# Kernel tuning notes

Measured on AMD Instinct MI355X. Metric: run time of the kernel, lower is better.

## Reference

```python
import jax, jax.numpy as jnp
import numpy as np

B, N = 2, 6
H, W = 64, 64            # BEV grid
FH, FW = 32, 88          # camera feature map
DIM, FEAT_DIM = 128, 128
HEADS, DH = 4, 32
QW1, QW2 = 8, 8          # query window
KW1, KW2 = 4, 11         # key/val window
IMG_H, IMG_W = 224, 480
EPS = 1e-5


def _ln(t, g, b):
    m = t.mean(-1, keepdims=True)
    v = ((t - m) ** 2).mean(-1, keepdims=True)
    return (t - m) / jnp.sqrt(v + EPS) * g + b


def _bn_relu_conv(t, g, b, Wc):
    # eval-mode BatchNorm2d (running_mean=0, running_var=1) -> ReLU -> 1x1 conv
    y = jax.nn.relu(t / jnp.sqrt(1.0 + EPS) * g[:, None, None] + b[:, None, None])
    return jnp.einsum('oc,nchw->nohw', Wc, y)


def _normalize(t, axis):
    n = jnp.sqrt(jnp.sum(t * t, axis=axis, keepdims=True))
    return t / jnp.maximum(n, 1e-12)


def _win(t, w1, w2):
    # (..., X*w1, Y*w2, d) -> (..., X, Y, w1, w2, d)
    s = t.shape
    t = t.reshape(*s[:-3], s[-3] // w1, w1, s[-2] // w2, w2, s[-1])
    return jnp.swapaxes(t, -4, -3)


def _unwin(t):
    # (..., X, Y, w1, w2, d) -> (..., X*w1, Y*w2, d)
    s = t.shape
    return jnp.swapaxes(t, -4, -3).reshape(*s[:-5], s[-5] * s[-3], s[-4] * s[-2], s[-1])


def _gridwin(t, w1, w2):
    bb, nn, Ht, Wt, d = t.shape
    t = t.reshape(bb, nn, w1, Ht // w1, w2, Wt // w2, d)
    return t.transpose(0, 1, 3, 5, 2, 4, 6)  # (b, n, X, Y, w1, w2, d)


def _cross_win_attn(qw, kw, vw, ln_g, ln_b, Wqkv, bqkv, Wp, bp, skip):
    b, n, X, Y, w1, w2, d = qw.shape
    f1, f2 = kw.shape[4], kw.shape[5]
    L = X * Y
    q = qw.transpose(0, 2, 3, 1, 4, 5, 6).reshape(b, L, n * w1 * w2, d)
    k = kw.transpose(0, 2, 3, 1, 4, 5, 6).reshape(b, L, n * f1 * f2, d)
    v = vw.transpose(0, 2, 3, 1, 4, 5, 6).reshape(b, L, n * f1 * f2, d)
    q = _ln(q, ln_g[0], ln_b[0]) @ Wqkv[0] + bqkv[0]
    k = _ln(k, ln_g[1], ln_b[1]) @ Wqkv[1] + bqkv[1]
    v = _ln(v, ln_g[2], ln_b[2]) @ Wqkv[2] + bqkv[2]
    split = lambda t: t.reshape(*t.shape[:-1], HEADS, DH)  # head-major channel split
    q, k, v = split(q), split(k), split(v)
    att = jax.nn.softmax(DH ** -0.5 * jnp.einsum('blqhd,blkhd->bhlqk', q, k), axis=-1)
    o = jnp.einsum('bhlqk,blkhd->blqhd', att, v).reshape(b, L, n * w1 * w2, HEADS * DH)
    o = o @ Wp + bp
    o = o.reshape(b, X, Y, n, w1, w2, d).mean(3)  # mean over cameras
    return o + skip


def _forward(x, grid, feature, I_inv, E_inv,
             bn_fl_g, bn_fl_b, W_fl, bn_fp_g, bn_fp_b, W_fp,
             W_bev, b_bev, W_img, W_cam,
             attn_ln_g, attn_ln_b, attn_Wqkv, attn_bqkv, attn_Wp, attn_bp,
             pn_g, pn_b, Wma, bma, Wmb, bmb, post_g, post_b):
    b, n = feature.shape[:2]
    # image plane (buffer)
    xs = jnp.linspace(0.0, 1.0, FW) * IMG_W
    ys = jnp.linspace(0.0, 1.0, FH) * IMG_H
    gx, gy = jnp.meshgrid(xs, ys)  # (FH, FW) each
    plane = jnp.stack([gx, gy, jnp.ones_like(gx)], 0).reshape(3, FH * FW)
    # camera embedding from translation column of E_inv
    c = E_inv[..., -1]                                   # (b, n, 4)
    c_embed = jnp.einsum('oc,bnc->bno', W_cam, c)        # (b, n, dim)
    # unprojected rays
    cam = jnp.einsum('bnij,jk->bnik', I_inv, plane)      # (b, n, 3, HW)
    cam = jnp.concatenate([cam, jnp.ones_like(cam[:, :, :1])], 2)
    d = jnp.einsum('bnij,bnjk->bnik', E_inv, cam)        # (b, n, 4, HW)
    d_img = d.reshape(b, n, 4, FH, FW)
    d_embed = jnp.einsum('oc,bnchw->bnohw', W_img, d_img)
    img_embed = _normalize(d_embed - c_embed[..., None, None], axis=2)
    # BEV positional embedding
    w_embed = jnp.einsum('oc,chw->ohw', W_bev, grid[:2]) + b_bev[:, None, None]
    bev_embed = _normalize(w_embed[None, None] - c_embed[..., None, None], axis=2)  # (b,n,dim,H,W)
    feat = feature.reshape(b * n, FEAT_DIM, FH, FW)
    key_im = img_embed + _bn_relu_conv(feat, bn_fp_g, bn_fp_b, W_fp).reshape(b, n, DIM, FH, FW)
    val_im = _bn_relu_conv(feat, bn_fl_g, bn_fl_b, W_fl).reshape(b, n, DIM, FH, FW)
    query = bev_embed + x[:, None]                       # (b, n, dim, H, W)
    # channel-last
    q_im = query.transpose(0, 1, 3, 4, 2)
    k_im = key_im.transpose(0, 1, 3, 4, 2)
    v_im = val_im.transpose(0, 1, 3, 4, 2)
    x_im = x.transpose(0, 2, 3, 1)
    # stage 1: local windows
    qw = _win(q_im, QW1, QW2)
    kw = _win(k_im, KW1, KW2)
    vw = _win(v_im, KW1, KW2)
    o1 = _cross_win_attn(qw, kw, vw, attn_ln_g[0], attn_ln_b[0], attn_Wqkv[0],
                         attn_bqkv[0], attn_Wp[0], attn_bp[0], _win(x_im, QW1, QW2))
    q1 = _unwin(o1)                                      # (b, H, W, d)
    q1 = q1 + jax.nn.gelu(_ln(q1, pn_g[0], pn_b[0]) @ Wma[0] + bma[0], approximate=False) @ Wmb[0] + bmb[0]
    # stage 2: grid (swapped) windows
    qg = jnp.broadcast_to(q1[:, None], (b, n) + q1.shape[1:])
    o2 = _cross_win_attn(_win(qg, QW1, QW2), _gridwin(k_im, KW1, KW2), _gridwin(v_im, KW1, KW2),
                         attn_ln_g[1], attn_ln_b[1], attn_Wqkv[1], attn_bqkv[1],
                         attn_Wp[1], attn_bp[1], _win(q1, QW1, QW2))
    q2 = _unwin(o2)
    q2 = q2 + jax.nn.gelu(_ln(q2, pn_g[1], pn_b[1]) @ Wma[1] + bma[1], approximate=False) @ Wmb[1] + bmb[1]
    out = _ln(q2, post_g, post_b)
    return out.transpose(0, 3, 1, 2)                     # (b, dim, H, W)


def setup_inputs() -> dict:
    key = jax.random.key(0)
    ks = jax.random.split(key, 16)
    rn = lambda i, shape, sc=0.02: jax.random.normal(ks[i], shape, dtype=jnp.float32) * sc
    return {
        'index': 0,
        'x': jax.random.normal(ks[0], (B, DIM, H, W), dtype=jnp.float32),
        'grid': jax.random.normal(ks[1], (2, H, W), dtype=jnp.float32),
        'feature': jax.random.normal(ks[2], (B, N, FEAT_DIM, FH, FW), dtype=jnp.float32),
        'I_inv': jax.random.normal(ks[3], (B, N, 3, 3), dtype=jnp.float32),
        'E_inv': jax.random.normal(ks[4], (B, N, 4, 4), dtype=jnp.float32),
        'bn_fl_g': jnp.ones((FEAT_DIM,), jnp.float32), 'bn_fl_b': jnp.zeros((FEAT_DIM,), jnp.float32),
        'W_fl': rn(5, (DIM, FEAT_DIM)),
        'bn_fp_g': jnp.ones((FEAT_DIM,), jnp.float32), 'bn_fp_b': jnp.zeros((FEAT_DIM,), jnp.float32),
        'W_fp': rn(6, (DIM, FEAT_DIM)),
        'W_bev': rn(7, (DIM, 2)), 'b_bev': jnp.zeros((DIM,), jnp.float32),
        'W_img': rn(8, (DIM, 4)), 'W_cam': rn(9, (DIM, 4)),
        'attn_ln_g': jnp.ones((2, 3, DIM), jnp.float32), 'attn_ln_b': jnp.zeros((2, 3, DIM), jnp.float32),
        'attn_Wqkv': rn(10, (2, 3, DIM, HEADS * DH)), 'attn_bqkv': jnp.zeros((2, 3, HEADS * DH), jnp.float32),
        'attn_Wp': rn(11, (2, HEADS * DH, DIM)), 'attn_bp': jnp.zeros((2, DIM), jnp.float32),
        'pn_g': jnp.ones((2, DIM), jnp.float32), 'pn_b': jnp.zeros((2, DIM), jnp.float32),
        'Wma': rn(12, (2, DIM, 2 * DIM)), 'bma': jnp.zeros((2, 2 * DIM), jnp.float32),
        'Wmb': rn(13, (2, 2 * DIM, DIM)), 'bmb': jnp.zeros((2, DIM), jnp.float32),
        'post_g': jnp.ones((DIM,), jnp.float32), 'post_b': jnp.zeros((DIM,), jnp.float32),
    }


def reference(index, x, grid, feature, I_inv, E_inv,
              bn_fl_g, bn_fl_b, W_fl, bn_fp_g, bn_fp_b, W_fp,
              W_bev, b_bev, W_img, W_cam,
              attn_ln_g, attn_ln_b, attn_Wqkv, attn_bqkv, attn_Wp, attn_bp,
              pn_g, pn_b, Wma, bma, Wmb, bmb, post_g, post_b):
    del index  # grid for this index is passed directly
    return _forward(x, grid, feature, I_inv, E_inv,
                    bn_fl_g, bn_fl_b, W_fl, bn_fp_g, bn_fp_b, W_fp,
                    W_bev, b_bev, W_img, W_cam,
                    attn_ln_g, attn_ln_b, attn_Wqkv, attn_bqkv, attn_Wp, attn_bp,
                    pn_g, pn_b, Wma, bma, Wmb, bmb, post_g, post_b)
```

## Files before the change

kernel.cpp:

```cpp
#include <hip/hip_runtime.h>
#include <math.h>


typedef __attribute__((ext_vector_type(8))) short short8;
typedef __attribute__((ext_vector_type(4))) float f32x4;

__device__ __forceinline__ unsigned short f2bf(float f){
  union { float f; unsigned u; } v; v.f = f;
  unsigned r = v.u + 0x7FFF + ((v.u >> 16) & 1);
  return (unsigned short)(r >> 16);
}
__device__ __forceinline__ float bf2f(unsigned short h){
  union { unsigned u; float f; } v; v.u = ((unsigned)h) << 16; return v.f;
}
__device__ __forceinline__ void store_bf16x8(unsigned short* p, const float* v){
  union { short8 s8; unsigned short u[8]; } u;
  #pragma unroll
  for (int i=0;i<8;i++) u.u[i] = f2bf(v[i]);
  *(short8*)p = u.s8;
}

__device__ __forceinline__ float gelu_erf(float x){
  float z = x * 0.70710678118654752f;
  float a = fabsf(z);
  float t = 1.0f / fmaf(0.3275911f, a, 1.0f);
  float p = t*(0.254829592f + t*(-0.284496736f + t*(1.421413741f +
            t*(-1.453152027f + t*1.061405429f))));
  float er = 1.0f - p*__expf(-a*a);
  er = copysignf(er, z);
  return 0.5f * x * (1.0f + er);
}

__device__ __forceinline__ size_t remap_kv(int tok, int mode){
  int bn = tok / 2816; int p = tok - bn*2816;
  int b = bn / 6, n = bn - b*6;
  int i = p / 88, j = p - i*88;
  int l, t;
  if (mode == 1){
    int jw = j / 11;
    l = (i >> 2)*8 + jw;
    t = n*44 + (i & 3)*11 + (j - jw*11);
  } else {
    l = (i & 7)*8 + (j & 7);
    t = n*44 + (i >> 3)*11 + (j >> 3);
  }
  return (size_t)((b*64 + l)*264 + t);
}

__global__ __launch_bounds__(256) void k_prepconv(
    const float* __restrict__ qkv, const float* __restrict__ wp,
    const float* __restrict__ wma, const float* __restrict__ wmb,
    unsigned short* __restrict__ Wt,
    const float* __restrict__ abqkv, float* __restrict__ biasP,
    const float* __restrict__ gridp, const float* __restrict__ Wbev,
    const float* __restrict__ bbev, const float* __restrict__ x,
    const float* __restrict__ lg, const float* __restrict__ lb,
    const float* __restrict__ Einv, const float* __restrict__ Wcam,
    unsigned short* __restrict__ Qh,
    const float* __restrict__ feat,
    const float* __restrict__ gfp, const float* __restrict__ bfp,
    const float* __restrict__ Wfp,
    const float* __restrict__ gfl, const float* __restrict__ bfl,
    const float* __restrict__ Wfl,
    const float* __restrict__ Iinv, const float* __restrict__ Wimg,
    unsigned short* __restrict__ K1h, unsigned short* __restrict__ V1h){
  constexpr int KP_ = 136;
  __shared__ unsigned short sW[128*KP_];
  __shared__ unsigned short sA[128*KP_];
  __shared__ float sg_[128], sb_[128];
  __shared__ float sMean[128], sRstd[128], sRn[128];
  __shared__ float sCE[128];
  __shared__ float4 sWI4[128];
  __shared__ float sIE[32];
  const int bid = blockIdx.x;
  const int tid = threadIdx.x;

  if (bid < 56){
    const int sel[14]  = {0,0,0,0,0,0, 1,1, 2,2, 3,3,3,3};
    const int soff[14] = {0,16384,32768,49152,65536,81920, 0,16384, 0,32768,
                          0,16384,32768,49152};
    const int doff[14] = {0,16384,32768,49152,65536,81920, 98304,114688,
                          131072,163840, 196608,212992,229376,245760};
    const int Ns[14]   = {128,128,128,128,128,128, 128,128, 256,256,
                          128,128,128,128};
    int sg = bid >> 2, q = bid & 3;
    const float* srcs[4] = {qkv, wp, wma, wmb};
    const float* src = srcs[sel[sg]] + soff[sg];
    unsigned short* dst = Wt + doff[sg];
    int K = 128, N = Ns[sg];
    int quarter = (K*N) >> 2;
    bool fold = (sg >= 1 && sg <= 5);
    const float* gv = lg + sg*128;
    for (int idx = q*quarter + tid; idx < (q+1)*quarter; idx += 256){
      int n = idx / K, k = idx - n*K;
      float v = src[k*N + n];
      if (fold) v *= gv[k];
      dst[idx] = f2bf(v);
    }
  } else if (bid < 62){
    if (tid < 128){
      int m = bid - 56;
      int n = tid;
      float s = abqkv[m*128 + n];
      if (m > 0){
        const float* lnb = lb + m*128;
        const float* W = qkv + m*16384;
        for (int k=0;k<128;k++) s = fmaf(lnb[k], W[k*128 + n], s);
      }
      biasP[m*128 + n] = s;
    }
  } else if (bid < 574){
    float* sx = (float*)sW;
    int bid2 = bid - 62;
    int b = bid2 >> 8; int pp0 = (bid2 & 255) << 4;
    {
      int cg = tid >> 4, px = tid & 15;
      #pragma unroll
      for (int i=0;i<8;i++){
        int c = cg + 16*i;
        sx[c*17 + px] = x[(size_t)b*524288 + (size_t)c*4096 + pp0 + px];
      }
    }
    __syncthreads();
    int xid = tid >> 4, part = tid & 15;
    int pix = pp0 + xid;
    int h = pix >> 6, w = pix & 63;
    int l = (h>>3)*8 + (w>>3);
    int tq = (h&7)*8 + (w&7);
    float g0 = gridp[pix], g1 = gridp[4096 + pix];
    float we[8], xv[8];
    #pragma unroll
    for (int k=0;k<8;k++){
      int o = part*8 + k;
      we[k] = Wbev[o*2]*g0 + Wbev[o*2+1]*g1 + bbev[o];
      xv[k] = sx[(part*8+k)*17 + xid];
    }
    for (int n=0; n<6; n++){
      const float* E = Einv + (b*6+n)*16;
      float v[8]; float sq = 0.f;
      #pragma unroll
      for (int k=0;k<8;k++){
        int o = part*8 + k;
        const float* Wc = Wcam + o*4;
        float ce = Wc[0]*E[3] + Wc[1]*E[7] + Wc[2]*E[11] + Wc[3]*E[15];
        float vv = we[k] - ce;
        v[k] = vv; sq = fmaf(vv, vv, sq);
      }
      #pragma unroll
      for (int off=8; off>0; off>>=1) sq += __shfl_xor(sq, off, 16);
      float rn = 1.0f / fmaxf(sqrtf(sq), 1e-12f);
      float q[8]; float s=0.f, s2=0.f;
      #pragma unroll
      for (int k=0;k<8;k++){
        q[k] = fmaf(v[k], rn, xv[k]);
        s += q[k]; s2 = fmaf(q[k], q[k], s2);
      }
      #pragma unroll
      for (int off=8; off>0; off>>=1){ s += __shfl_xor(s, off, 16); s2 += __shfl_xor(s2, off, 16); }
      float mean = s*(1.f/128.f);
      float rstd = rsqrtf(fmaxf(s2*(1.f/128.f) - mean*mean, 0.f) + 1e-5f);
      size_t row = (size_t)((b*64 + l)*384 + n*64 + tq);
      float o8[8];
      #pragma unroll
      for (int k=0;k<8;k++){
        int c = part*8 + k;
        o8[k] = fmaf((q[k]-mean)*rstd, lg[c], lb[c]);
      }
      store_bf16x8(Qh + row*128 + part*8, o8);
    }
  } else {
    const int bid2c = bid - 574;
    const int which = (bid2c >= 264);
    const int cbid = which ? bid2c - 264 : bid2c;
    const float* gg = which ? gfl : gfp;
    const float* bb = which ? bfl : bfp;
    const float* Wf = which ? Wfl : Wfp;
    unsigned short* OUT = which ? V1h : K1h;
    const int base = cbid * 128;
    const int bn = base / 2816;
    const int pbase = base - bn*2816;
    for (int i = tid; i < 2048; i += 256){
      int n = i >> 4, k8 = (i & 15) << 3;
      const float* wsp = Wf + (size_t)n*128 + k8;
      float4 f0 = *(const float4*)wsp;
      float4 f1 = *(const float4*)(wsp+4);
      float v8[8] = {f0.x,f0.y,f0.z,f0.w,f1.x,f1.y,f1.z,f1.w};
      store_bf16x8(&sW[n*KP_ + k8], v8);
    }
    if (tid < 128){ sg_[tid]=gg[tid]; sb_[tid]=bb[tid]; }
    if (!which){
      if (tid < 128){
        const float* E = Einv + bn*16;
        float4 wc = *(const float4*)(Wcam + tid*4);
        sCE[tid] = wc.x*E[3] + wc.y*E[7] + wc.z*E[11] + wc.w*E[15];
        sWI4[tid] = *(const float4*)(Wimg + tid*4);
      }
      if (tid < 25) sIE[tid] = (tid < 9) ? Iinv[bn*9 + tid] : Einv[bn*16 + (tid-9)];
    }
    const float RSQ = rsqrtf(1.0f + 1e-5f);
    {
      int prow = tid & 127, cseg = tid >> 7;
      int p = pbase + prow;
      const float* fb = feat + ((size_t)bn*128 + cseg*64)*2816 + p;
      #pragma unroll 8
      for (int i=0;i<64;i+=2){
        int c = cseg*64 + i;
        float t0 = fb[(size_t)i*2816] * RSQ;
        float t1 = fb[(size_t)(i+1)*2816] * RSQ;
        float y0 = fmaxf(fmaf(t0, sg_[c],   sb_[c]),   0.f);
        float y1 = fmaxf(fmaf(t1, sg_[c+1], sb_[c+1]), 0.f);
        unsigned u = (unsigned)f2bf(y0) | ((unsigned)f2bf(y1) << 16);
        *(unsigned*)&sA[prow*KP_ + c] = u;
      }
    }
    __syncthreads();
    const int lane = tid & 63, wv = tid >> 6;
    const int lane15 = lane & 15, quad = lane >> 4;
    const int n0 = wv * 32;
    f32x4 acc[8][2];
    #pragma unroll
    for (int mt=0; mt<8; mt++){ acc[mt][0]=(f32x4)0.f; acc[mt][1]=(f32x4)0.f; }
    const unsigned short* aptr = sA + lane15*KP_ + quad*8;
    const unsigned short* bptr = sW + (size_t)(n0 + lane15)*KP_ + quad*8;
    #pragma unroll
    for (int kk=0; kk<4; kk++){
      short8 af[8], bf2v[2];
      #pragma unroll
      for (int mt=0; mt<8; mt++) af[mt] = *(const short8*)(aptr + mt*16*KP_ + kk*32);
      bf2v[0] = *(const short8*)(bptr + kk*32);
      bf2v[1] = *(const short8*)(bptr + 16*KP_ + kk*32);
      #pragma unroll
      for (int mt=0; mt<8; mt++){
        acc[mt][0] = __builtin_amdgcn_mfma_f32_16x16x32_bf16(af[mt], bf2v[0], acc[mt][0], 0,0,0);
        acc[mt][1] = __builtin_amdgcn_mfma_f32_16x16x32_bf16(af[mt], bf2v[1], acc[mt][1], 0,0,0);
      }
    }
    __syncthreads();
    if (!which){
      const int r = tid >> 1, half = tid & 1;
      int p = pbase + r;
      int ii = p / 88, jj = p - ii*88;
      float xs = (float)jj * (480.0f/87.0f);
      float ys = (float)ii * (224.0f/31.0f);
      float c0 = sIE[0]*xs + sIE[1]*ys + sIE[2];
      float c1 = sIE[3]*xs + sIE[4]*ys + sIE[5];
      float c2 = sIE[6]*xs + sIE[7]*ys + sIE[8];
      float d0 = sIE[9]*c0  + sIE[10]*c1 + sIE[11]*c2 + sIE[12];
      float d1 = sIE[13]*c0 + sIE[14]*c1 + sIE[15]*c2 + sIE[16];
      float d2 = sIE[17]*c0 + sIE[18]*c1 + sIE[19]*c2 + sIE[20];
      float d3 = sIE[21]*c0 + sIE[22]*c1 + sIE[23]*c2 + sIE[24];
      float sq = 0.f;
      #pragma unroll 8
      for (int k=0;k<64;k++){
        int c = half*64 + k;
        float4 w = sWI4[c];
        float de = w.x*d0 + w.y*d1 + w.z*d2 + w.w*d3 - sCE[c];
        sA[r*KP_ + c] = f2bf(de);
        sq = fmaf(de, de, sq);
      }
      sq += __shfl_xor(sq, 1);
      if (half == 0) sRn[r] = 1.0f / fmaxf(sqrtf(sq), 1e-12f);
    }
    __syncthreads();
    #pragma unroll
    for (int mt=0; mt<8; mt++){
      #pragma unroll
      for (int nt=0; nt<2; nt++){
        int col = n0 + nt*16 + lane15;
        #pragma unroll
        for (int r4=0; r4<4; r4++){
          int row = mt*16 + quad*4 + r4;
          float v = acc[mt][nt][r4];
          if (!which) v += bf2f(sA[row*KP_ + col]) * sRn[row];
          sA[row*KP_ + col] = f2bf(v);
        }
      }
    }
    __syncthreads();
    {
      int r = tid >> 1, part = tid & 1;
      float s=0.f, s2=0.f;
      #pragma unroll 8
      for (int k=0;k<64;k++){
        float v = bf2f(sA[r*KP_ + part*64 + k]);
        s += v; s2 = fmaf(v,v,s2);
      }
      s += __shfl_xor(s, 1); s2 += __shfl_xor(s2, 1);
      if (part == 0){
        float mean = s*(1.f/128.f);
        sMean[r] = mean;
        sRstd[r] = rsqrtf(fmaxf(s2*(1.f/128.f) - mean*mean, 0.f) + 1e-5f);
      }
    }
    __syncthreads();
    for (int i = tid; i < 2048; i += 256){
      int row = i >> 4, seg = i & 15;
      float mean = sMean[row], rstd = sRstd[row];
      union { short8 s; unsigned short u[8]; } t;
      t.s = *(const short8*)&sA[row*KP_ + seg*8];
      float v[8];
      #pragma unroll
      for (int k=0;k<8;k++) v[k] = (bf2f(t.u[k]) - mean)*rstd;
      store_bf16x8(OUT + (size_t)(base+row)*128 + seg*8, v);
    }
  }
}

struct GArg {
  const unsigned short* Xh;
  const unsigned short* Wt; const float* bias;
  unsigned short* OUTH; float oscale; int outmode;
};
struct G5 { GArg g[5]; int s[4]; };

__global__ __launch_bounds__(256) void k_qkv5(G5 A){
  constexpr int KP_ = 136;
  __shared__ unsigned short sW[128*KP_];
  __shared__ unsigned short sA[128*KP_];
  __shared__ float sbias[128];
  const int b0 = (int)blockIdx.x;
  const int ridx = (b0 < A.s[0]) ? 0 : (b0 < A.s[1]) ? 1 : (b0 < A.s[2]) ? 2
                 : (b0 < A.s[3]) ? 3 : 4;
  const GArg g = A.g[ridx];
  const int bid = b0 - (ridx ? A.s[ridx-1] : 0);
  const int base = bid * 128;
  const int tid = threadIdx.x;
  for (int i = tid; i < 2048; i += 256){
    int n = i >> 4, k8 = (i & 15) << 3;
    *(short8*)&sW[n*KP_ + k8] = *(const short8*)(g.Wt + (size_t)n*128 + k8);
  }
  if (tid < 128) sbias[tid] = g.bias[tid];
  {
    const int r = tid >> 1, part = tid & 1;
    const short8* src = (const short8*)(g.Xh + (size_t)(base+r)*128 + part*64);
    short8* dst = (short8*)(sA + r*KP_ + part*64);
    #pragma unroll
    for (int k=0;k<8;k++) dst[k] = src[k];
  }
  __syncthreads();
  const int lane = tid & 63, wv = tid >> 6;
  const int lane15 = lane & 15, quad = lane >> 4;
  const int n0 = wv * 32;
  f32x4 acc[8][2];
  #pragma unroll
  for (int mt=0; mt<8; mt++){ acc[mt][0]=(f32x4)0.f; acc[mt][1]=(f32x4)0.f; }
  const unsigned short* aptr = sA + lane15*KP_ + quad*8;
  const unsigned short* bptr = sW + (size_t)(n0 + lane15)*KP_ + quad*8;
  #pragma unroll
  for (int kk=0; kk<4; kk++){
    short8 af[8], bf2v[2];
    #pragma unroll
    for (int mt=0; mt<8; mt++) af[mt] = *(const short8*)(aptr + mt*16*KP_ + kk*32);
    bf2v[0] = *(const short8*)(bptr + kk*32);
    bf2v[1] = *(const short8*)(bptr + 16*KP_ + kk*32);
    #pragma unroll
    for (int mt=0; mt<8; mt++){
      acc[mt][0] = __builtin_amdgcn_mfma_f32_16x16x32_bf16(af[mt], bf2v[0], acc[mt][0], 0,0,0);
      acc[mt][1] = __builtin_amdgcn_mfma_f32_16x16x32_bf16(af[mt], bf2v[1], acc[mt][1], 0,0,0);
    }
  }
  __syncthreads();
  #pragma unroll
  for (int mt=0; mt<8; mt++){
    #pragma unroll
    for (int nt=0; nt<2; nt++){
      int col = n0 + nt*16 + lane15;
      float bsv = sbias[col];
      #pragma unroll
      for (int r4=0; r4<4; r4++){
        int row = mt*16 + quad*4 + r4;
        sA[row*KP_ + col] = f2bf((acc[mt][nt][r4] + bsv) * g.oscale);
      }
    }
  }
  __syncthreads();
  for (int i = tid; i < 2048; i += 256){
    int row = i >> 4, seg = i & 15;
    int rrow = base + row;
    size_t orow = g.outmode ? remap_kv(rrow, g.outmode) : (size_t)rrow;
    *(short8*)(g.OUTH + orow*128 + seg*8) = *(const short8*)&sA[row*KP_ + seg*8];
  }
}

__global__ __launch_bounds__(256) void k_tail(
    const unsigned short* __restrict__ AOh,
    const float* __restrict__ skipf, int skipmode,
    const unsigned short* __restrict__ WtP, const float* __restrict__ abp,
    const float* __restrict__ png, const float* __restrict__ pnb,
    const unsigned short* __restrict__ WtMAa, const unsigned short* __restrict__ WtMAb,
    const float* __restrict__ bma,
    const unsigned short* __restrict__ WtMBa, const unsigned short* __restrict__ WtMBb,
    const float* __restrict__ bmb,
    float* __restrict__ Q1out,
    const unsigned short* __restrict__ WtQ2, const float* __restrict__ q2bias,
    float q2scale, unsigned short* __restrict__ QPout,
    const float* __restrict__ postg, const float* __restrict__ postb,
    float* __restrict__ out){
  constexpr int KP_ = 136;
  __shared__ unsigned short sW[128*KP_];
  __shared__ unsigned short sX[32*KP_];
  __shared__ unsigned short sH1[32*KP_];
  __shared__ unsigned short sH2[32*KP_];
  __shared__ float sCUR[32*132];
  __shared__ float sbias[128];
  __shared__ float sg[128], sb2[128];
  __shared__ float sMean[32], sRstd[32];
  const int tid = threadIdx.x;
  const int base = blockIdx.x * 32;
  const int lane = tid & 63, wv = tid >> 6;
  const int lane15 = lane & 15, quad = lane >> 4;
  const int n0 = wv * 32;

  auto loadW = [&](const unsigned short* Wp){
    for (int i = tid; i < 2048; i += 256){
      int n = i >> 4, k8 = (i & 15) << 3;
      *(short8*)&sW[n*KP_ + k8] = *(const short8*)(Wp + (size_t)n*128 + k8);
    }
  };
  auto domfma = [&](const unsigned short* Asrc, f32x4 acc[2][2]){
    const unsigned short* aptr = Asrc + lane15*KP_ + quad*8;
    const unsigned short* bptr = sW + (size_t)(n0 + lane15)*KP_ + quad*8;
    #pragma unroll
    for (int kk=0; kk<4; kk++){
      short8 a0 = *(const short8*)(aptr + kk*32);
      short8 a1 = *(const short8*)(aptr + 16*KP_ + kk*32);
      short8 b0 = *(const short8*)(bptr + kk*32);
      short8 b1 = *(const short8*)(bptr + 16*KP_ + kk*32);
      acc[0][0] = __builtin_amdgcn_mfma_f32_16x16x32_bf16(a0,b0,acc[0][0],0,0,0);
      acc[1][0] = __builtin_amdgcn_mfma_f32_16x16x32_bf16(a1,b0,acc[1][0],0,0,0);
      acc[0][1] = __builtin_amdgcn_mfma_f32_16x16x32_bf16(a0,b1,acc[0][1],0,0,0);
      acc[1][1] = __builtin_amdgcn_mfma_f32_16x16x32_bf16(a1,b1,acc[1][1],0,0,0);
    }
  };

  loadW(WtP);
  {
    const int r = tid >> 3, part = tid & 7;
    const short8* src = (const short8*)(AOh + (size_t)(base+r)*128 + part*16);
    short8* dst = (short8*)(sX + r*KP_ + part*16);
    dst[0] = src[0]; dst[1] = src[1];
  }
  if (tid < 128){ sbias[tid] = abp[tid]; sg[tid] = png[tid]; sb2[tid] = pnb[tid]; }
  __syncthreads();
  {
    f32x4 acc[2][2];
    acc[0][0]=(f32x4)0.f; acc[0][1]=(f32x4)0.f;
    acc[1][0]=(f32x4)0.f; acc[1][1]=(f32x4)0.f;
    domfma(sX, acc);
    #pragma unroll
    for (int mt=0; mt<2; mt++)
      #pragma unroll
      for (int nt=0; nt<2; nt++){
        int col = n0 + nt*16 + lane15;
        float bsv = sbias[col];
        #pragma unroll
        for (int r4=0; r4<4; r4++){
          int row = mt*16 + quad*4 + r4;
          int rrow = base + row;
          float v = acc[mt][nt][r4] + bsv;
          if (skipmode == 1){
            int bb = rrow >> 12, l = (rrow >> 6) & 63, pp = rrow & 63;
            int pix = (((l>>3)*8 + (pp>>3)) << 6) + (l&7)*8 + (pp&7);
            v += skipf[(size_t)bb*524288 + (size_t)col*4096 + pix];
          } else {
            v += skipf[(size_t)rrow*128 + col];
          }
          sCUR[row*132 + col] = v;
        }
      }
  }
  __syncthreads();
  loadW(WtMAa);
  if (tid < 128) sbias[tid] = bma[tid];
  {
    const int r = tid >> 3, part = tid & 7;
    float v[16];
    #pragma unroll
    for (int k=0;k<16;k++) v[k] = sCUR[r*132 + part*16 + k];
    float s=0.f, s2=0.f;
    #pragma unroll
    for (int k=0;k<16;k++){ s += v[k]; s2 = fmaf(v[k],v[k],s2); }
    #pragma unroll
    for (int off=4; off>0; off>>=1){ s += __shfl_xor(s, off, 8); s2 += __shfl_xor(s2, off, 8); }
    float mean = s*(1.f/128.f);
    float rstd = rsqrtf(fmaxf(s2*(1.f/128.f) - mean*mean, 0.f) + 1e-5f);
    #pragma unroll
    for (int k=0;k<16;k++){
      int c = part*16 + k;
      v[k] = fmaf((v[k]-mean)*rstd, sg[c], sb2[c]);
    }
    store_bf16x8(sX + r*KP_ + part*16, v);
    store_bf16x8(sX + r*KP_ + part*16 + 8, v+8);
  }
  __syncthreads();
  {
    f32x4 acc[2][2];
    acc[0][0]=(f32x4)0.f; acc[0][1]=(f32x4)0.f;
    acc[1][0]=(f32x4)0.f; acc[1][1]=(f32x4)0.f;
    domfma(sX, acc);
    #pragma unroll
    for (int mt=0; mt<2; mt++)
      #pragma unroll
      for (int nt=0; nt<2; nt++){
        int col = n0 + nt*16 + lane15;
        float bsv = sbias[col];
        #pragma unroll
        for (int r4=0; r4<4; r4++){
          int row = mt*16 + quad*4 + r4;
          sH1[row*KP_ + col] = f2bf(gelu_erf(acc[mt][nt][r4] + bsv));
        }
      }
  }
  __syncthreads();
  loadW(WtMAb);
  if (tid < 128) sbias[tid] = bma[128 + tid];
  __syncthreads();
  {
    f32x4 acc[2][2];
    acc[0][0]=(f32x4)0.f; acc[0][1]=(f32x4)0.f;
    acc[1][0]=(f32x4)0.f; acc[1][1]=(f32x4)0.f;
    domfma(sX, acc);
    #pragma unroll
    for (int mt=0; mt<2; mt++)
      #pragma unroll
      for (int nt=0; nt<2; nt++){
        int col = n0 + nt*16 + lane15;
        float bsv = sbias[col];
        #pragma unroll
        for (int r4=0; r4<4; r4++){
          int row = mt*16 + quad*4 + r4;
          sH2[row*KP_ + col] = f2bf(gelu_erf(acc[mt][nt][r4] + bsv));
        }
      }
  }
  __syncthreads();
  loadW(WtMBa);
  if (tid < 128) sbias[tid] = bmb[tid];
  __syncthreads();
  f32x4 acc[2][2];
  acc[0][0]=(f32x4)0.f; acc[0][1]=(f32x4)0.f;
  acc[1][0]=(f32x4)0.f; acc[1][1]=(f32x4)0.f;
  domfma(sH1, acc);
  __syncthreads();
  loadW(WtMBb);
  __syncthreads();
  domfma(sH2, acc);
  if (out == nullptr){
    #pragma unroll
    for (int mt=0; mt<2; mt++)
      #pragma unroll
      for (int nt=0; nt<2; nt++){
        int col = n0 + nt*16 + lane15;
        float bsv = sbias[col];
        #pragma unroll
        for (int r4=0; r4<4; r4++){
          int row = mt*16 + quad*4 + r4;
          float v = acc[mt][nt][r4] + bsv + sCUR[row*132 + col];
          sCUR[row*132 + col] = v;
          Q1out[(size_t)(base+row)*128 + col] = v;
        }
      }
    __syncthreads();
    {
      const int r = tid >> 3, part = tid & 7;
      float s=0.f, s2=0.f;
      #pragma unroll
      for (int k=0;k<16;k++){
        float v = sCUR[r*132 + part*16 + k];
        s += v; s2 = fmaf(v,v,s2);
      }
      #pragma unroll
      for (int off=4; off>0; off>>=1){ s += __shfl_xor(s, off, 8); s2 += __shfl_xor(s2, off, 8); }
      if (part == 0){
        float mean = s*(1.f/128.f);
        sMean[r] = mean;
        sRstd[r] = rsqrtf(fmaxf(s2*(1.f/128.f) - mean*mean, 0.f) + 1e-5f);
      }
    }
    __syncthreads();
    {
      const int r = tid >> 3, part = tid & 7;
      float mean = sMean[r], rstd = sRstd[r];
      float v[16];
      #pragma unroll
      for (int k=0;k<16;k++) v[k] = (sCUR[r*132 + part*16 + k] - mean)*rstd;
      store_bf16x8(sX + r*KP_ + part*16, v);
      store_bf16x8(sX + r*KP_ + part*16 + 8, v+8);
    }
    loadW(WtQ2);
    if (tid < 128) sbias[tid] = q2bias[tid];
    __syncthreads();
    f32x4 a2[2][2];
    a2[0][0]=(f32x4)0.f; a2[0][1]=(f32x4)0.f;
    a2[1][0]=(f32x4)0.f; a2[1][1]=(f32x4)0.f;
    domfma(sX, a2);
    #pragma unroll
    for (int mt=0; mt<2; mt++)
      #pragma unroll
      for (int nt=0; nt<2; nt++){
        int col = n0 + nt*16 + lane15;
        float bsv = sbias[col];
        #pragma unroll
        for (int r4=0; r4<4; r4++){
          int row = mt*16 + quad*4 + r4;
          sH1[row*KP_ + col] = f2bf((a2[mt][nt][r4] + bsv) * q2scale);
        }
      }
    __syncthreads();
    for (int i = tid; i < 512; i += 256){
      int row = i >> 4, seg = i & 15;
      *(short8*)(QPout + (size_t)(base+row)*128 + seg*8) = *(const short8*)&sH1[row*KP_ + seg*8];
    }
  } else {
    float res[2][2][4];
    #pragma unroll
    for (int mt=0; mt<2; mt++)
      #pragma unroll
      for (int nt=0; nt<2; nt++){
        int col = n0 + nt*16 + lane15;
        float bsv = sbias[col];
        #pragma unroll
        for (int r4=0; r4<4; r4++){
          int row = mt*16 + quad*4 + r4;
          res[mt][nt][r4] = acc[mt][nt][r4] + bsv + sCUR[row*132 + col];
        }
      }
    __syncthreads();
    #pragma unroll
    for (int mt=0; mt<2; mt++)
      #pragma unroll
      for (int nt=0; nt<2; nt++){
        int col = n0 + nt*16 + lane15;
        #pragma unroll
        for (int r4=0; r4<4; r4++){
          int row = mt*16 + quad*4 + r4;
          sCUR[row*132 + col] = res[mt][nt][r4];
        }
      }
    __syncthreads();
    {
      const int r = tid >> 3, part = tid & 7;
      float s=0.f, s2=0.f;
      #pragma unroll
      for (int k=0;k<16;k++){
        float v = sCUR[r*132 + part*16 + k];
        s += v; s2 = fmaf(v,v,s2);
      }
      #pragma unroll
      for (int off=4; off>0; off>>=1){ s += __shfl_xor(s, off, 8); s2 += __shfl_xor(s2, off, 8); }
      if (part == 0){
        float mean = s*(1.f/128.f);
        sMean[r] = mean;
        sRstd[r] = rsqrtf(fmaxf(s2*(1.f/128.f) - mean*mean, 0.f) + 1e-5f);
      }
    }
    __syncthreads();
    {
      int c = tid & 127, half = tid >> 7;
      int b = base >> 12, l = (base >> 6) & 63, p0 = base & 63;
      float go = postg[c], bo = postb[c];
      #pragma unroll
      for (int seg=0; seg<2; seg++){
        int p = p0 + half*16 + seg*8;
        int hrow = (l>>3)*8 + (p>>3);
        int w0 = (l&7)*8;
        float rr[8];
        #pragma unroll
        for (int j=0;j<8;j++){
          int row = half*16 + seg*8 + j;
          rr[j] = fmaf((sCUR[row*132 + c] - sMean[row])*sRstd[row], go, bo);
        }
        size_t obase = ((size_t)(b*128 + c))*4096 + (size_t)hrow*64 + w0;
        *(float4*)&out[obase]   = make_float4(rr[0],rr[1],rr[2],rr[3]);
        *(float4*)&out[obase+4] = make_float4(rr[4],rr[5],rr[6],rr[7]);
      }
    }
  }
}

__global__ __launch_bounds__(256) void k_attn2(const unsigned short* __restrict__ QPh,
    const unsigned short* __restrict__ KPh, const unsigned short* __restrict__ VPh,
    unsigned short* __restrict__ AOh, int nrep, int nQ){
  __shared__ unsigned short Ksh[288*40];
  __shared__ unsigned short Vt[32*296];
  __shared__ unsigned short Psh[4*16*40];
  __shared__ float rs[4*16];
  int hd = blockIdx.x & 3; int bl = blockIdx.x >> 2;
  size_t kvbase = (size_t)bl*264;
  int tid = threadIdx.x;
  for (int idx = tid; idx < 1056; idx += 256){
    int row = idx >> 2, seg = idx & 3;
    *(short8*)&Ksh[row*40 + seg*8] =
      *(const short8*)(KPh + (kvbase+row)*128 + hd*32 + seg*8);
  }
  for (int idx = tid; idx < 96; idx += 256){
    int row = 264 + (idx>>2), seg = idx & 3;
    short8 z = {0,0,0,0,0,0,0,0};
    *(short8*)&Ksh[row*40 + seg*8] = z;
  }
  for (int idx = tid; idx < 528; idx += 256){
    int kp = idx >> 2, seg = idx & 3;
    union { short8 s; unsigned short u[8]; } a, b;
    a.s = *(const short8*)(VPh + (kvbase + 2*kp)*128 + hd*32 + seg*8);
    b.s = *(const short8*)(VPh + (kvbase + 2*kp + 1)*128 + hd*32 + seg*8);
    #pragma unroll
    for (int i=0;i<8;i++)
      *(unsigned*)&Vt[(seg*8+i)*296 + 2*kp] = (unsigned)a.u[i] | ((unsigned)b.u[i] << 16);
  }
  for (int idx = tid; idx < 384; idx += 256){
    int d = idx / 12, kp = 264 + (idx % 12)*2;
    *(unsigned*)&Vt[d*296 + kp] = 0u;
  }
  __syncthreads();
  const int wv = tid >> 6, lane = tid & 63;
  const int lane15 = lane & 15, quad = lane >> 4;
  unsigned short* Pw = Psh + wv*640;
  float* rsw = rs + wv*16;
  short8 vfrag[9][2];
  #pragma unroll
  for (int kc=0; kc<9; kc++){
    vfrag[kc][0] = *(const short8*)&Vt[(lane15)*296      + kc*32 + quad*8];
    vfrag[kc][1] = *(const short8*)&Vt[(16+lane15)*296   + kc*32 + quad*8];
  }
  f32x4 macc0 = (f32x4)0.f, macc1 = (f32x4)0.f;
  for (int cam = 0; cam < nrep; cam++){
    int qrow = bl*nQ + (cam*4 + wv)*16 + lane15;
    short8 qf = *(const short8*)(QPh + (size_t)qrow*128 + hd*32 + quad*8);
    f32x4 oa0 = (f32x4)0.f, oa1 = (f32x4)0.f;
    float rsum = 0.f;
    #pragma unroll
    for (int kc=0; kc<9; kc++){
      #pragma unroll
      for (int sub=0; sub<2; sub++){
        int kt = kc*2 + sub;
        short8 kf = *(const short8*)&Ksh[(kt*16 + lane15)*40 + quad*8];
        f32x4 st = __builtin_amdgcn_mfma_f32_16x16x32_bf16(kf, qf, (f32x4)0.f, 0,0,0);
        int kbase = kt*16 + quad*4;
        float e0 = (kbase+0 < 264) ? __expf(st[0]) : 0.f;
        float e1 = (kbase+1 < 264) ? __expf(st[1]) : 0.f;
        float e2 = (kbase+2 < 264) ? __expf(st[2]) : 0.f;
        float e3 = (kbase+3 < 264) ? __expf(st[3]) : 0.f;
        rsum += (e0+e1)+(e2+e3);
        uint2 pk;
        pk.x = (unsigned)f2bf(e0) | ((unsigned)f2bf(e1) << 16);
        pk.y = (unsigned)f2bf(e2) | ((unsigned)f2bf(e3) << 16);
        *(uint2*)&Pw[lane15*40 + sub*16 + quad*4] = pk;
      }
      short8 pf = *(const short8*)&Pw[lane15*40 + quad*8];
      oa0 = __builtin_amdgcn_mfma_f32_16x16x32_bf16(pf, vfrag[kc][0], oa0, 0,0,0);
      oa1 = __builtin_amdgcn_mfma_f32_16x16x32_bf16(pf, vfrag[kc][1], oa1, 0,0,0);
    }
    rsum += __shfl_xor(rsum, 16);
    rsum += __shfl_xor(rsum, 32);
    if (lane < 16) rsw[lane] = rsum;
    f32x4 rv = *(f32x4*)&rsw[quad*4];
    #pragma unroll
    for (int r=0;r<4;r++){
      float inv = 1.f / rv[r];
      macc0[r] = fmaf(oa0[r], inv, macc0[r]);
      macc1[r] = fmaf(oa1[r], inv, macc1[r]);
    }
  }
  float sc = (nrep == 6) ? (1.f/6.f) : 1.f;
  int pixb = wv*16 + quad*4;
  #pragma unroll
  for (int r=0;r<4;r++){
    size_t rowo = ((size_t)(bl*64 + pixb + r))*128 + hd*32;
    AOh[rowo + lane15]      = f2bf(macc0[r]*sc);
    AOh[rowo + 16 + lane15] = f2bf(macc1[r]*sc);
  }
}

extern "C" void kernel_launch(void* const* d_in, const int* in_sizes, int n_in,
                              void* d_out, int out_size, void* d_ws, size_t ws_size,
                              hipStream_t stream) {
  (void)in_sizes; (void)n_in; (void)out_size; (void)ws_size;
  const float* x     = (const float*)d_in[1];
  const float* gridp = (const float*)d_in[2];
  const float* feat  = (const float*)d_in[3];
  const float* Iinv  = (const float*)d_in[4];
  const float* Einv  = (const float*)d_in[5];
  const float* gfl   = (const float*)d_in[6];
  const float* bfl   = (const float*)d_in[7];
  const float* Wfl   = (const float*)d_in[8];
  const float* gfp   = (const float*)d_in[9];
  const float* bfp   = (const float*)d_in[10];
  const float* Wfp   = (const float*)d_in[11];
  const float* Wbev  = (const float*)d_in[12];
  const float* bbev  = (const float*)d_in[13];
  const float* Wimg  = (const float*)d_in[14];
  const float* Wcam  = (const float*)d_in[15];
  const float* alng  = (const float*)d_in[16];
  const float* alnb  = (const float*)d_in[17];
  const float* aWqkv = (const float*)d_in[18];
  const float* abqkv = (const float*)d_in[19];
  const float* aWp   = (const float*)d_in[20];
  const float* abp   = (const float*)d_in[21];
  const float* png   = (const float*)d_in[22];
  const float* pnb   = (const float*)d_in[23];
  const float* Wma   = (const float*)d_in[24];
  const float* bma   = (const float*)d_in[25];
  const float* Wmb   = (const float*)d_in[26];
  const float* bmb   = (const float*)d_in[27];
  const float* postg = (const float*)d_in[28];
  const float* postb = (const float*)d_in[29];
  float* out = (float*)d_out;
  float* ws  = (float*)d_ws;
  const float QSC = 0.17677669529663687f;

  float* biasP = ws;
  unsigned short* Wt   = (unsigned short*)(ws + 2048);
  unsigned short* K1h  = (unsigned short*)(ws + 149504);
  unsigned short* V1h  = K1h + 4325376;
  unsigned short* KPh  = V1h + 4325376;
  unsigned short* VPh  = KPh + 4325376;
  unsigned short* KP2h = VPh + 4325376;
  unsigned short* VP2h = KP2h + 4325376;
  unsigned short* QPh  = VP2h + 4325376;
  unsigned short* Qbh  = QPh + 6291456;
  unsigned short* AOh  = Qbh + 6291456;
  float* Q1f = (float*)(AOh + 1048576);

  unsigned short* WtQ1 = Wt;            unsigned short* WtK1 = Wt + 16384;
  unsigned short* WtV1 = Wt + 32768;    unsigned short* WtQ2 = Wt + 49152;
  unsigned short* WtK2 = Wt + 65536;    unsigned short* WtV2 = Wt + 81920;
  unsigned short* WtP1 = Wt + 98304;    unsigned short* WtP2 = Wt + 114688;
  unsigned short* WtMA1 = Wt + 131072;  unsigned short* WtMA2 = Wt + 163840;
  unsigned short* WtMB1a = Wt + 196608; unsigned short* WtMB1b = Wt + 212992;
  unsigned short* WtMB2a = Wt + 229376; unsigned short* WtMB2b = Wt + 245760;

  k_prepconv<<<1102, 256, 0, stream>>>(aWqkv, aWp, Wma, Wmb, Wt,
      abqkv, biasP, gridp, Wbev, bbev, x, alng, alnb, Einv, Wcam, Qbh,
      feat, gfp, bfp, Wfp, gfl, bfl, Wfl, Iinv, Wimg, K1h, V1h);

  {
    G5 A;
    A.g[0] = GArg{Qbh, WtQ1, biasP,      QPh,  QSC, 0};
    A.g[1] = GArg{K1h, WtK1, biasP+128,  KPh,  1.f, 1};
    A.g[2] = GArg{V1h, WtV1, biasP+256,  VPh,  1.f, 1};
    A.g[3] = GArg{K1h, WtK2, biasP+512,  KP2h, 1.f, 2};
    A.g[4] = GArg{V1h, WtV2, biasP+640,  VP2h, 1.f, 2};
    A.s[0] = 384; A.s[1] = 648; A.s[2] = 912; A.s[3] = 1176;
    k_qkv5<<<1440, 256, 0, stream>>>(A);
  }
  k_attn2<<<512, 256, 0, stream>>>(QPh, KPh, VPh, AOh, 6, 384);
  k_tail<<<256, 256, 0, stream>>>(AOh, x, 1, WtP1, abp, png, pnb,
      WtMA1, WtMA1+16384, bma, WtMB1a, WtMB1b, bmb, Q1f,
      WtQ2, biasP+384, QSC, QPh,
      nullptr, nullptr, nullptr);
  k_attn2<<<512, 256, 0, stream>>>(QPh, KP2h, VP2h, AOh, 1, 64);
  k_tail<<<256, 256, 0, stream>>>(AOh, Q1f, 3, WtP2, abp+128, png+128, pnb+128,
      WtMA2, WtMA2+16384, bma+256, WtMB2a, WtMB2b, bmb+128, nullptr,
      nullptr, nullptr, 0.f, nullptr,
      postg, postb, out);
}
```

Baseline: 254.1 us.

## Fuse Q projection into prep kernel and share K/V tile across two projections

The first-stage Q projection GEMM moves into the prep kernel. Each block converts the Q weight to bf16 in shared memory and runs MFMA on its 96 freshly normalized query rows, so the Qbh intermediate is no longer written to and read back from global memory. The K/V projection kernel now loads each K1/V1 tile once and applies both the stage-1 and stage-2 weights to it, halving activation reads and block count. The cost is that every prep block re-converts the full 128x128 fp32 weight, and the prep blocks carry more shared memory and registers.

Measured after the change: 255.8 us. About the same (+0.7%).

```diff
diff --git a/kernel.cpp b/kernel.cpp
--- a/kernel.cpp
+++ b/kernel.cpp
@@ -56,7 +56,7 @@
     const float* __restrict__ bbev, const float* __restrict__ x,
     const float* __restrict__ lg, const float* __restrict__ lb,
     const float* __restrict__ Einv, const float* __restrict__ Wcam,
-    unsigned short* __restrict__ Qh,
+    unsigned short* __restrict__ QPh,
     const float* __restrict__ feat,
     const float* __restrict__ gfp, const float* __restrict__ bfp,
     const float* __restrict__ Wfp,
@@ -67,21 +67,17 @@
   constexpr int KP_ = 136;
   __shared__ unsigned short sW[128*KP_];
   __shared__ unsigned short sA[128*KP_];
-  __shared__ float sg_[128], sb_[128];
-  __shared__ float sMean[128], sRstd[128], sRn[128];
-  __shared__ float sCE[128];
-  __shared__ float4 sWI4[128];
-  __shared__ float sIE[32];
+  __shared__ __align__(16) float sMisc[2560];
   const int bid = blockIdx.x;
   const int tid = threadIdx.x;
 
-  if (bid < 56){
-    const int sel[14]  = {0,0,0,0,0,0, 1,1, 2,2, 3,3,3,3};
-    const int soff[14] = {0,16384,32768,49152,65536,81920, 0,16384, 0,32768,
+  if (bid < 52){
+    const int sel[13]  = {0,0,0,0,0, 1,1, 2,2, 3,3,3,3};
+    const int soff[13] = {16384,32768,49152,65536,81920, 0,16384, 0,32768,
                           0,16384,32768,49152};
-    const int doff[14] = {0,16384,32768,49152,65536,81920, 98304,114688,
+    const int doff[13] = {16384,32768,49152,65536,81920, 98304,114688,
                           131072,163840, 196608,212992,229376,245760};
-    const int Ns[14]   = {128,128,128,128,128,128, 128,128, 256,256,
+    const int Ns[13]   = {128,128,128,128,128, 128,128, 256,256,
                           128,128,128,128};
     int sg = bid >> 2, q = bid & 3;
     const float* srcs[4] = {qkv, wp, wma, wmb};
@@ -89,17 +85,17 @@
     unsigned short* dst = Wt + doff[sg];
     int K = 128, N = Ns[sg];
     int quarter = (K*N) >> 2;
-    bool fold = (sg >= 1 && sg <= 5);
-    const float* gv = lg + sg*128;
+    bool fold = (sg <= 4);
+    const float* gv = lg + (sg+1)*128;
     for (int idx = q*quarter + tid; idx < (q+1)*quarter; idx += 256){
       int n = idx / K, k = idx - n*K;
       float v = src[k*N + n];
       if (fold) v *= gv[k];
       dst[idx] = f2bf(v);
     }
-  } else if (bid < 62){
+  } else if (bid < 58){
     if (tid < 128){
-      int m = bid - 56;
+      int m = bid - 52;
       int n = tid;
       float s = abqkv[m*128 + n];
       if (m > 0){
@@ -109,10 +105,16 @@
       }
       biasP[m*128 + n] = s;
     }
-  } else if (bid < 574){
-    float* sx = (float*)sW;
-    int bid2 = bid - 62;
+  } else if (bid < 570){
+    const float QSCALE = 0.17677669529663687f;
+    float* sx = sMisc;
+    int* rowoff = (int*)(sMisc + 2176);
+    int bid2 = bid - 58;
     int b = bid2 >> 8; int pp0 = (bid2 & 255) << 4;
+    for (int idx = tid; idx < 16384; idx += 256){
+      int n = idx & 127, k = idx >> 7;
+      sW[n*KP_ + k] = f2bf(qkv[(size_t)k*128 + n]);
+    }
     {
       int cg = tid >> 4, px = tid & 15;
       #pragma unroll
@@ -121,12 +123,14 @@
         sx[c*17 + px] = x[(size_t)b*524288 + (size_t)c*4096 + pp0 + px];
       }
     }
+    if (tid < 16){
+      int pix = pp0 + tid; int h = pix >> 6, w = pix & 63;
+      int l = (h>>3)*8 + (w>>3); int tq = (h&7)*8 + (w&7);
+      rowoff[tid] = (b*64 + l)*384 + tq;
+    }
     __syncthreads();
     int xid = tid >> 4, part = tid & 15;
     int pix = pp0 + xid;
-    int h = pix >> 6, w = pix & 63;
-    int l = (h>>3)*8 + (w>>3);
-    int tq = (h&7)*8 + (w&7);
     float g0 = gridp[pix], g1 = gridp[4096 + pix];
     float we[8], xv[8];
     #pragma unroll
@@ -159,17 +163,66 @@
       for (int off=8; off>0; off>>=1){ s += __shfl_xor(s, off, 16); s2 += __shfl_xor(s2, off, 16); }
       float mean = s*(1.f/128.f);
       float rstd = rsqrtf(fmaxf(s2*(1.f/128.f) - mean*mean, 0.f) + 1e-5f);
-      size_t row = (size_t)((b*64 + l)*384 + n*64 + tq);
       float o8[8];
       #pragma unroll
       for (int k=0;k<8;k++){
         int c = part*8 + k;
         o8[k] = fmaf((q[k]-mean)*rstd, lg[c], lb[c]);
       }
-      store_bf16x8(Qh + row*128 + part*8, o8);
+      store_bf16x8(sA + (size_t)(n*16 + xid)*KP_ + part*8, o8);
+    }
+    __syncthreads();
+    const int lane = tid & 63, wv = tid >> 6;
+    const int lane15 = lane & 15, quad = lane >> 4;
+    const int n0 = wv * 32;
+    f32x4 acc[6][2];
+    #pragma unroll
+    for (int mt=0; mt<6; mt++){ acc[mt][0]=(f32x4)0.f; acc[mt][1]=(f32x4)0.f; }
+    const unsigned short* aptr = sA + lane15*KP_ + quad*8;
+    const unsigned short* bptr = sW + (size_t)(n0 + lane15)*KP_ + quad*8;
+    #pragma unroll
+    for (int kk=0; kk<4; kk++){
+      short8 af[6], bf2v[2];
+      #pragma unroll
+      for (int mt=0; mt<6; mt++) af[mt] = *(const short8*)(aptr + mt*16*KP_ + kk*32);
+      bf2v[0] = *(const short8*)(bptr + kk*32);
+      bf2v[1] = *(const short8*)(bptr + 16*KP_ + kk*32);
+      #pragma unroll
+      for (int mt=0; mt<6; mt++){
+        acc[mt][0] = __builtin_amdgcn_mfma_f32_16x16x32_bf16(af[mt], bf2v[0], acc[mt][0], 0,0,0);
+        acc[mt][1] = __builtin_amdgcn_mfma_f32_16x16x32_bf16(af[mt], bf2v[1], acc[mt][1], 0,0,0);
+      }
+    }
+    __syncthreads();
+    #pragma unroll
+    for (int nt=0; nt<2; nt++){
+      int col = n0 + nt*16 + lane15;
+      float bsv = abqkv[col];
+      #pragma unroll
+      for (int mt=0; mt<6; mt++){
+        #pragma unroll
+        for (int r4=0; r4<4; r4++){
+          int row = mt*16 + quad*4 + r4;
+          sA[row*KP_ + col] = f2bf((acc[mt][nt][r4] + bsv) * QSCALE);
+        }
+      }
+    }
+    __syncthreads();
+    for (int i = tid; i < 1536; i += 256){
+      int r = i >> 4, seg = i & 15;
+      size_t grow = (size_t)rowoff[r & 15] + (r >> 4)*64;
+      *(short8*)(QPh + grow*128 + seg*8) = *(const short8*)&sA[r*KP_ + seg*8];
     }
   } else {
-    const int bid2c = bid - 574;
+    float* sg_  = sMisc;
+    float* sb_  = sMisc + 128;
+    float* sMean= sMisc + 256;
+    float* sRstd= sMisc + 384;
+    float* sRn  = sMisc + 512;
+    float* sCE  = sMisc + 640;
+    float4* sWI4= (float4*)(sMisc + 768);
+    float* sIE  = sMisc + 1280;
+    const int bid2c = bid - 570;
     const int which = (bid2c >= 264);
     const int cbid = which ? bid2c - 264 : bid2c;
     const float* gg = which ? gfl : gfp;
@@ -306,46 +359,49 @@
   }
 }
 
-struct GArg {
-  const unsigned short* Xh;
-  const unsigned short* Wt; const float* bias;
-  unsigned short* OUTH; float oscale; int outmode;
-};
-struct G5 { GArg g[5]; int s[4]; };
-
-__global__ __launch_bounds__(256) void k_qkv5(G5 A){
+__global__ __launch_bounds__(256) void k_kvdual(
+    const unsigned short* __restrict__ K1h, const unsigned short* __restrict__ V1h,
+    const unsigned short* __restrict__ WtK1, const unsigned short* __restrict__ WtK2,
+    const unsigned short* __restrict__ WtV1, const unsigned short* __restrict__ WtV2,
+    const float* __restrict__ biasP,
+    unsigned short* __restrict__ KPh, unsigned short* __restrict__ KP2h,
+    unsigned short* __restrict__ VPh, unsigned short* __restrict__ VP2h){
   constexpr int KP_ = 136;
   __shared__ unsigned short sW[128*KP_];
   __shared__ unsigned short sA[128*KP_];
   __shared__ float sbias[128];
-  const int b0 = (int)blockIdx.x;
-  const int ridx = (b0 < A.s[0]) ? 0 : (b0 < A.s[1]) ? 1 : (b0 < A.s[2]) ? 2
-                 : (b0 < A.s[3]) ? 3 : 4;
-  const GArg g = A.g[ridx];
-  const int bid = b0 - (ridx ? A.s[ridx-1] : 0);
-  const int base = bid * 128;
+  const int which = (blockIdx.x >= 264);
+  const int cbid = which ? blockIdx.x - 264 : blockIdx.x;
+  const int base = cbid * 128;
+  const unsigned short* Xh = which ? V1h : K1h;
+  const unsigned short* Wa = which ? WtV1 : WtK1;
+  const unsigned short* Wb = which ? WtV2 : WtK2;
+  unsigned short* Oa = which ? VPh : KPh;
+  unsigned short* Ob = which ? VP2h : KP2h;
+  const float* ba = biasP + (which ? 256 : 128);
+  const float* bb = biasP + (which ? 640 : 512);
   const int tid = threadIdx.x;
   for (int i = tid; i < 2048; i += 256){
     int n = i >> 4, k8 = (i & 15) << 3;
-    *(short8*)&sW[n*KP_ + k8] = *(const short8*)(g.Wt + (size_t)n*128 + k8);
-  }
-  if (tid < 128) sbias[tid] = g.bias[tid];
+    *(short8*)&sW[n*KP_ + k8] = *(const short8*)(Wa + (size_t)n*128 + k8);
+  }
   {
     const int r = tid >> 1, part = tid & 1;
-    const short8* src = (const short8*)(g.Xh + (size_t)(base+r)*128 + part*64);
+    const short8* src = (const short8*)(Xh + (size_t)(base+r)*128 + part*64);
     short8* dst = (short8*)(sA + r*KP_ + part*64);
     #pragma unroll
     for (int k=0;k<8;k++) dst[k] = src[k];
   }
+  if (tid < 128) sbias[tid] = ba[tid];
   __syncthreads();
   const int lane = tid & 63, wv = tid >> 6;
   const int lane15 = lane & 15, quad = lane >> 4;
   const int n0 = wv * 32;
+  const unsigned short* aptr = sA + lane15*KP_ + quad*8;
+  const unsigned short* bptr = sW + (size_t)(n0 + lane15)*KP_ + quad*8;
   f32x4 acc[8][2];
   #pragma unroll
   for (int mt=0; mt<8; mt++){ acc[mt][0]=(f32x4)0.f; acc[mt][1]=(f32x4)0.f; }
-  const unsigned short* aptr = sA + lane15*KP_ + quad*8;
-  const unsigned short* bptr = sW + (size_t)(n0 + lane15)*KP_ + quad*8;
   #pragma unroll
   for (int kk=0; kk<4; kk++){
     short8 af[8], bf2v[2];
@@ -369,16 +425,57 @@
       #pragma unroll
       for (int r4=0; r4<4; r4++){
         int row = mt*16 + quad*4 + r4;
-        sA[row*KP_ + col] = f2bf((acc[mt][nt][r4] + bsv) * g.oscale);
+        sW[row*KP_ + col] = f2bf(acc[mt][nt][r4] + bsv);
       }
     }
   }
   __syncthreads();
   for (int i = tid; i < 2048; i += 256){
     int row = i >> 4, seg = i & 15;
-    int rrow = base + row;
-    size_t orow = g.outmode ? remap_kv(rrow, g.outmode) : (size_t)rrow;
-    *(short8*)(g.OUTH + orow*128 + seg*8) = *(const short8*)&sA[row*KP_ + seg*8];
+    size_t orow = remap_kv(base + row, 1);
+    *(short8*)(Oa + orow*128 + seg*8) = *(const short8*)&sW[row*KP_ + seg*8];
+  }
+  if (tid < 128) sbias[tid] = bb[tid];
+  __syncthreads();
+  for (int i = tid; i < 2048; i += 256){
+    int n = i >> 4, k8 = (i & 15) << 3;
+    *(short8*)&sW[n*KP_ + k8] = *(const short8*)(Wb + (size_t)n*128 + k8);
+  }
+  __syncthreads();
+  #pragma unroll
+  for (int mt=0; mt<8; mt++){ acc[mt][0]=(f32x4)0.f; acc[mt][1]=(f32x4)0.f; }
+  #pragma unroll
+  for (int kk=0; kk<4; kk++){
+    short8 af[8], bf2v[2];
+    #pragma unroll
+    for (int mt=0; mt<8; mt++) af[mt] = *(const short8*)(aptr + mt*16*KP_ + kk*32);
+    bf2v[0] = *(const short8*)(bptr + kk*32);
+    bf2v[1] = *(const short8*)(bptr + 16*KP_ + kk*32);
+    #pragma unroll
+    for (int mt=0; mt<8; mt++){
+      acc[mt][0] = __builtin_amdgcn_mfma_f32_16x16x32_bf16(af[mt], bf2v[0], acc[mt][0], 0,0,0);
+      acc[mt][1] = __builtin_amdgcn_mfma_f32_16x16x32_bf16(af[mt], bf2v[1], acc[mt][1], 0,0,0);
+    }
+  }
+  __syncthreads();
+  #pragma unroll
+  for (int mt=0; mt<8; mt++){
+    #pragma unroll
+    for (int nt=0; nt<2; nt++){
+      int col = n0 + nt*16 + lane15;
+      float bsv = sbias[col];
+      #pragma unroll
+      for (int r4=0; r4<4; r4++){
+        int row = mt*16 + quad*4 + r4;
+        sA[row*KP_ + col] = f2bf(acc[mt][nt][r4] + bsv);
+      }
+    }
+  }
+  __syncthreads();
+  for (int i = tid; i < 2048; i += 256){
+    int row = i >> 4, seg = i & 15;
+    size_t orow = remap_kv(base + row, 2);
+    *(short8*)(Ob + orow*128 + seg*8) = *(const short8*)&sA[row*KP_ + seg*8];
   }
 }
 
@@ -821,7 +918,7 @@
   unsigned short* AOh  = Qbh + 6291456;
   float* Q1f = (float*)(AOh + 1048576);
 
-  unsigned short* WtQ1 = Wt;            unsigned short* WtK1 = Wt + 16384;
+  unsigned short* WtK1 = Wt + 16384;
   unsigned short* WtV1 = Wt + 32768;    unsigned short* WtQ2 = Wt + 49152;
   unsigned short* WtK2 = Wt + 65536;    unsigned short* WtV2 = Wt + 81920;
   unsigned short* WtP1 = Wt + 98304;    unsigned short* WtP2 = Wt + 114688;
@@ -829,20 +926,13 @@
   unsigned short* WtMB1a = Wt + 196608; unsigned short* WtMB1b = Wt + 212992;
   unsigned short* WtMB2a = Wt + 229376; unsigned short* WtMB2b = Wt + 245760;
 
-  k_prepconv<<<1102, 256, 0, stream>>>(aWqkv, aWp, Wma, Wmb, Wt,
-      abqkv, biasP, gridp, Wbev, bbev, x, alng, alnb, Einv, Wcam, Qbh,
+  k_prepconv<<<1098, 256, 0, stream>>>(aWqkv, aWp, Wma, Wmb, Wt,
+      abqkv, biasP, gridp, Wbev, bbev, x, alng, alnb, Einv, Wcam, QPh,
       feat, gfp, bfp, Wfp, gfl, bfl, Wfl, Iinv, Wimg, K1h, V1h);
 
-  {
-    G5 A;
-    A.g[0] = GArg{Qbh, WtQ1, biasP,      QPh,  QSC, 0};
-    A.g[1] = GArg{K1h, WtK1, biasP+128,  KPh,  1.f, 1};
-    A.g[2] = GArg{V1h, WtV1, biasP+256,  VPh,  1.f, 1};
-    A.g[3] = GArg{K1h, WtK2, biasP+512,  KP2h, 1.f, 2};
-    A.g[4] = GArg{V1h, WtV2, biasP+640,  VP2h, 1.f, 2};
-    A.s[0] = 384; A.s[1] = 648; A.s[2] = 912; A.s[3] = 1176;
-    k_qkv5<<<1440, 256, 0, stream>>>(A);
-  }
+  k_kvdual<<<528, 256, 0, stream>>>(K1h, V1h, WtK1, WtK2, WtV1, WtV2,
+      biasP, KPh, KP2h, VPh, VP2h);
+
   k_attn2<<<512, 256, 0, stream>>>(QPh, KPh, VPh, AOh, 6, 384);
   k_tail<<<256, 256, 0, stream>>>(AOh, x, 1, WtP1, abp, png, pnb,
       WtMA1, WtMA1+16384, bma, WtMB1a, WtMB1b, bmb, Q1f,
```
